# Kernel optimization log

Measured on AMD Instinct MI355X. Metric: run time of the kernel, lower is better.

## Reference

```python
import jax, jax.numpy as jnp
import numpy as np
from jax import lax

DN = ('NCHW', 'OIHW', 'NCHW')

def _conv(x, w, b, pad):
    y = lax.conv_general_dilated(x, w, (1, 1), pad, dimension_numbers=DN)
    return y + b[None, :, None, None]

def _squash(u, eps=1e-8):
    sn = jnp.sum(u * u, axis=1, keepdims=True)  # channel-dim squared norm
    return (sn / (1.0 + sn)) * u / (jnp.sqrt(sn) + eps)

def _expert(x, w_caps, b_caps, w_proj, b_proj):
    # 16 stacked 3x3 capsule convs == one 3x3 conv 128->128 (same concat order)
    u = _conv(x, w_caps, b_caps, 'SAME')
    u = _squash(u)
    return _conv(u, w_proj, b_proj, [(0, 0), (0, 0)])

def _process_gate(x, expert_all, g, top):
    B = x.shape[0]
    x0 = x.mean(axis=(2, 3))                          # [B, C] GAP
    gate_out = jax.nn.softmax(x0 @ g, axis=1)         # [B, E]
    usage = gate_out.sum(0)                           # [E]
    tw, ti = lax.top_k(gate_out, top)                 # [B, top]
    tw = jax.nn.softmax(tw, axis=1)
    sel = expert_all[ti, jnp.arange(B)[:, None]]      # [B, top, C, H, W]
    y = jnp.sum(sel * tw[:, :, None, None, None], axis=1)
    loss = jnp.var(usage, ddof=1) / (usage.mean() ** 2 + 1e-10)
    return y, loss

def setup_inputs() -> dict:
    key = jax.random.key(0)
    ks = jax.random.split(key, 8)
    B, C, H, W, E = 8, 128, 64, 64, 8
    fan_g = 1.0 / np.sqrt(C)
    return {
        'x': jax.random.normal(ks[0], (B, C, H, W), jnp.float32),
        'gate1': jax.random.normal(ks[1], (C, E), jnp.float32) * fan_g,
        'gate2': jax.random.normal(ks[2], (C, E), jnp.float32) * fan_g,
        'gate3': jax.random.normal(ks[3], (C, E), jnp.float32) * fan_g,
        'gate4': jax.random.normal(ks[4], (C, E), jnp.float32) * fan_g,
        'W_caps': jax.random.normal(ks[5], (E, C, C, 3, 3), jnp.float32) * (1.0 / np.sqrt(C * 9)),
        'b_caps': jnp.zeros((E, C), jnp.float32),
        'W_proj': jax.random.normal(ks[6], (E, C, C, 1, 1), jnp.float32) * (1.0 / np.sqrt(C)),
        'b_proj': jnp.zeros((E, C), jnp.float32),
    }

def reference(x, gate1, gate2, gate3, gate4, W_caps, b_caps, W_proj, b_proj):
    top = 2
    # Expert outputs are gate-independent: compute each expert on the full batch once.
    expert_all = jax.vmap(lambda wc, bc, wp, bp: _expert(x, wc, bc, wp, bp))(
        W_caps, b_caps, W_proj, b_proj)      # [E, B, C, H, W]
    y1, l1 = _process_gate(x, expert_all, gate1, top)
    y2, l2 = _process_gate(x, expert_all, gate2, top)
    y3, l3 = _process_gate(x, expert_all, gate3, top)
    y4, l4 = _process_gate(x, expert_all, gate4, top)
    return (y1, y2, y3, y4, l1 + l2 + l3 + l4)
```

## Files before the change

kernel.cpp:

```cpp
#include <hip/hip_runtime.h>
#include <math.h>

#define B_   8
#define C_   128
#define E_   8
#define HW_  4096

typedef unsigned short u16;
typedef unsigned int   u32;
typedef __attribute__((ext_vector_type(8))) short bf16x8;
typedef __attribute__((ext_vector_type(4))) float f32x4;

__device__ __forceinline__ u16 f2bf(float f) {
  u32 u = __float_as_uint(f);
  u32 r = (u + 0x7fffu + ((u >> 16) & 1u)) >> 16;
  return (u16)r;
}
__device__ __forceinline__ float bf2f(u16 h) {
  return __uint_as_float(((u32)h) << 16);
}
__device__ __forceinline__ void gld_lds16(const u16* g, u16* l) {
  __builtin_amdgcn_global_load_lds((const __attribute__((address_space(1))) u32*)g,
                                   (__attribute__((address_space(3))) u32*)(void*)l,
                                   16, 0, 0);
}
#define MFMA(a, b, c) __builtin_amdgcn_mfma_f32_16x16x32_bf16(a, b, c, 0, 0, 0)

__global__ __launch_bounds__(256) void k_mean(const float* __restrict__ x,
                                              float* __restrict__ x0) {
  int bc = blockIdx.x;
  const float4* p = (const float4*)(x + (size_t)bc * HW_);
  float s = 0.f;
  for (int i = threadIdx.x; i < HW_ / 4; i += 256) {
    float4 v = p[i];
    s += v.x + v.y + v.z + v.w;
  }
#pragma unroll
  for (int off = 32; off > 0; off >>= 1) s += __shfl_down(s, off);
  __shared__ float red[4];
  if ((threadIdx.x & 63) == 0) red[threadIdx.x >> 6] = s;
  __syncthreads();
  if (threadIdx.x == 0)
    x0[bc] = (red[0] + red[1] + red[2] + red[3]) * (1.f / HW_);
}

__global__ __launch_bounds__(256) void k_gate(const float* __restrict__ x0,
    const float* __restrict__ g1, const float* __restrict__ g2,
    const float* __restrict__ g3, const float* __restrict__ g4,
    float* __restrict__ wmat, float* __restrict__ w2, int* __restrict__ idxb,
    int* __restrict__ needed, float* __restrict__ lossp) {
  __shared__ float go[4][8][8];
  int t = threadIdx.x;
  int g = t >> 6, b = (t >> 3) & 7, e = t & 7;
  const float* gp = (g == 0) ? g1 : (g == 1) ? g2 : (g == 2) ? g3 : g4;
  const float* xr = x0 + b * C_;
  float s = 0.f;
  for (int c = 0; c < C_; ++c) s += xr[c] * gp[c * E_ + e];
  go[g][b][e] = s;
  wmat[t] = 0.f;
  if (t < 64) needed[t] = 0;
  __syncthreads();
  if (t < 32) {
    int gg = t >> 3, bb = t & 7;
    float m = -1e30f;
#pragma unroll
    for (int k = 0; k < 8; ++k) m = fmaxf(m, go[gg][bb][k]);
    float tmp[8]; float sum = 0.f;
#pragma unroll
    for (int k = 0; k < 8; ++k) { tmp[k] = expf(go[gg][bb][k] - m); sum += tmp[k]; }
    float inv = 1.f / sum;
#pragma unroll
    for (int k = 0; k < 8; ++k) { tmp[k] *= inv; go[gg][bb][k] = tmp[k]; }
    float v0 = -1.f; int i0 = 0;
#pragma unroll
    for (int k = 0; k < 8; ++k) if (tmp[k] > v0) { v0 = tmp[k]; i0 = k; }
    float v1 = -1.f; int i1 = 0;
#pragma unroll
    for (int k = 0; k < 8; ++k) if (k != i0 && tmp[k] > v1) { v1 = tmp[k]; i1 = k; }
    float e1 = expf(v1 - v0);
    float w0 = 1.f / (1.f + e1), w1 = e1 / (1.f + e1);
    w2[t * 2] = w0; w2[t * 2 + 1] = w1;
    idxb[t * 2] = i0; idxb[t * 2 + 1] = i1;
    wmat[(gg * 8 + bb) * 8 + i0] = w0;
    wmat[(gg * 8 + bb) * 8 + i1] = w1;
    needed[i0 * 8 + bb] = 1;
    needed[i1 * 8 + bb] = 1;
  }
  __syncthreads();
  if (t == 0) {
    float total = 0.f;
    for (int gg = 0; gg < 4; ++gg) {
      float us[8]; float mean = 0.f;
      for (int k = 0; k < 8; ++k) {
        float u = 0.f;
        for (int bb = 0; bb < 8; ++bb) u += go[gg][bb][k];
        us[k] = u; mean += u;
      }
      mean *= 0.125f;
      float var = 0.f;
      for (int k = 0; k < 8; ++k) { float d = us[k] - mean; var += d * d; }
      var *= (1.f / 7.f);
      total += var / (mean * mean + 1e-10f);
    }
    *lossp = total;
  }
}

__global__ __launch_bounds__(256) void k_prepx(const float* __restrict__ x,
                                               u16* __restrict__ XTh,
                                               u16* __restrict__ XTl) {
  int y = blockIdx.x;
  int b = blockIdx.y;
  __shared__ float T[64 * 129];
  for (int i = threadIdx.x; i < 128 * 64; i += 256) {
    int ci = i >> 6, xc = i & 63;
    T[xc * 129 + ci] = x[((size_t)(b * 128 + ci)) * HW_ + y * 64 + xc];
  }
  __syncthreads();
  for (int i = threadIdx.x; i < 64 * 128; i += 256) {
    int xc = i >> 7, ci = i & 127;
    float v = T[xc * 129 + ci];
    u16 h = f2bf(v);
    size_t o = ((size_t)(b * HW_ + y * 64 + xc)) * 128 + ci;
    XTh[o] = h;
    XTl[o] = f2bf(v - bf2f(h));
  }
}

__global__ __launch_bounds__(256) void k_prepw(const float* __restrict__ Wc,
    const float* __restrict__ Wp, u16* __restrict__ Wph, u16* __restrict__ Wpl,
    u16* __restrict__ Pph, u16* __restrict__ Ppl) {
  int gid = blockIdx.x * 256 + threadIdx.x;
  int stride = gridDim.x * 256;
  const int N1 = 8 * 9 * 2 * 128 * 64;
  for (int g = gid; g < N1; g += stride) {
    int k = g & 63;
    int co = (g >> 6) & 127;
    int ch = (g >> 13) & 1;
    int v = g >> 14;
    int tap = v % 9, e = v / 9;
    int ci = ch * 64 + k;
    float wv = Wc[(((size_t)(e * 128 + co)) * 128 + ci) * 9 + tap];
    u16 h = f2bf(wv), lo = f2bf(wv - bf2f(h));
    int idx = (v * 2 + ch) * 8192 + co * 64 + (k ^ ((co & 7) << 3));
    Wph[idx] = h; Wpl[idx] = lo;
  }
  const int N2 = 8 * 4 * 128 * 32;
  for (int g = gid; g < N2; g += stride) {
    int k = g & 31;
    int co = (g >> 5) & 127;
    int c = (g >> 12) & 3;
    int e = g >> 14;
    int ci = c * 32 + k;
    float wv = Wp[((size_t)(e * 128 + co)) * 128 + ci];
    u16 h = f2bf(wv), lo = f2bf(wv - bf2f(h));
    int idx = (e * 4 + c) * 4096 + co * 32 + (k ^ ((co & 3) << 3));
    Pph[idx] = h; Ppl[idx] = lo;
  }
}

__global__ __launch_bounds__(256, 2) void k_expert(
    const u16* __restrict__ XTh, const u16* __restrict__ XTl,
    const u16* __restrict__ Wph, const u16* __restrict__ Wpl,
    const u16* __restrict__ Pph, const u16* __restrict__ Ppl,
    const float* __restrict__ bcap, const float* __restrict__ bproj,
    const int* __restrict__ needed, const float* __restrict__ wmat,
    float* __restrict__ expb, float* __restrict__ yout, int use_exp) {
  int e = blockIdx.z, b = blockIdx.y;
  if (!needed[e * 8 + b]) return;
  int tile = blockIdx.x;
  int y0 = tile * 2;

  __shared__ __align__(16) char smem[75264];
  u16* S = (u16*)smem;
  const int Ah = 0, Al = 8192, Bh = 16384, Bl = 24576;
  const int Vh = 0, Vl = 16384, Pt = 32768;
  float* snb = (float*)(smem + 73728);
  float* fb  = (float*)(smem + 74752);

  int tid = threadIdx.x;
  int lane = tid & 63, w = tid >> 6;
  int l15 = lane & 15, l4 = lane >> 4;
  int cob = (w >> 1) * 64, nb = (w & 1) * 64;

  f32x4 zero4 = {0.f, 0.f, 0.f, 0.f};
  f32x4 acc[4][4];
#pragma unroll
  for (int i = 0; i < 4; ++i)
#pragma unroll
    for (int j = 0; j < 4; ++j) acc[i][j] = zero4;

  int sn_ = tid >> 1;
  int kh = (tid & 1) * 4;
  int srow = y0 + (sn_ >> 6);
  int scol = sn_ & 63;

  for (int tap = 0; tap < 9; ++tap) {
    int dy = tap / 3 - 1, dx = tap % 3 - 1;
    int row = srow + dy, col = scol + dx;
    bool val = ((unsigned)row < 64u) && ((unsigned)col < 64u);
    int gidx = val ? ((b * HW_ + row * 64 + col) * 128) : 0;
    for (int ch = 0; ch < 2; ++ch) {
      __syncthreads();
      const u16* wsh = Wph + (size_t)(((e * 9 + tap) * 2 + ch)) * 8192;
      const u16* wsl = Wpl + (size_t)(((e * 9 + tap) * 2 + ch)) * 8192;
#pragma unroll
      for (int q = 0; q < 4; ++q) {
        int off = (w * 4 + q) * 512;
        gld_lds16(wsh + off + lane * 8, S + Ah + off);
        gld_lds16(wsl + off + lane * 8, S + Al + off);
      }
      int ci0 = ch * 64;
#pragma unroll
      for (int i = 0; i < 4; ++i) {
        int kg = kh + i;
        uint4 vh4 = {0u, 0u, 0u, 0u}, vl4 = {0u, 0u, 0u, 0u};
        if (val) {
          vh4 = *(const uint4*)(XTh + gidx + ci0 + kg * 8);
          vl4 = *(const uint4*)(XTl + gidx + ci0 + kg * 8);
        }
        int wa = sn_ * 64 + ((kg * 8) ^ ((sn_ & 7) << 3));
        *(uint4*)(S + Bh + wa) = vh4;
        *(uint4*)(S + Bl + wa) = vl4;
      }
      __syncthreads();
#pragma unroll
      for (int ks = 0; ks < 2; ++ks) {
        bf16x8 fah[4], fal[4], fbh[4], fbl[4];
#pragma unroll
        for (int i = 0; i < 4; ++i) {
          int co = cob + i * 16 + l15;
          int ka = (ks * 32 + l4 * 8) ^ ((co & 7) << 3);
          fah[i] = *(const bf16x8*)(S + Ah + co * 64 + ka);
          fal[i] = *(const bf16x8*)(S + Al + co * 64 + ka);
        }
#pragma unroll
        for (int j = 0; j < 4; ++j) {
          int pn = nb + j * 16 + l15;
          int kb = (ks * 32 + l4 * 8) ^ ((pn & 7) << 3);
          fbh[j] = *(const bf16x8*)(S + Bh + pn * 64 + kb);
          fbl[j] = *(const bf16x8*)(S + Bl + pn * 64 + kb);
        }
#pragma unroll
        for (int i = 0; i < 4; ++i)
#pragma unroll
          for (int j = 0; j < 4; ++j) {
            acc[i][j] = MFMA(fah[i], fbh[j], acc[i][j]);
            acc[i][j] = MFMA(fah[i], fbl[j], acc[i][j]);
            acc[i][j] = MFMA(fal[i], fbh[j], acc[i][j]);
          }
      }
    }
  }

#pragma unroll
  for (int i = 0; i < 4; ++i)
#pragma unroll
    for (int r = 0; r < 4; ++r) {
      float bc = bcap[e * 128 + cob + i * 16 + l4 * 4 + r];
#pragma unroll
      for (int j = 0; j < 4; ++j) acc[i][j][r] += bc;
    }

#pragma unroll
  for (int j = 0; j < 4; ++j) {
    float p = 0.f;
#pragma unroll
    for (int i = 0; i < 4; ++i)
#pragma unroll
      for (int r = 0; r < 4; ++r) p += acc[i][j][r] * acc[i][j][r];
    p += __shfl_xor(p, 16);
    p += __shfl_xor(p, 32);
    if (lane < 16) snb[(w >> 1) * 128 + nb + j * 16 + lane] = p;
  }
  __syncthreads();
  if (tid < 128) {
    float s2 = snb[tid] + snb[128 + tid];
    fb[tid] = s2 / ((1.f + s2) * (sqrtf(s2) + 1e-8f));
  }
  __syncthreads();

#pragma unroll
  for (int j = 0; j < 4; ++j) {
    int pn = nb + j * 16 + l15;
    float fj = fb[pn];
#pragma unroll
    for (int i = 0; i < 4; ++i) {
      int co0v = cob + i * 16 + l4 * 4;
      float v0 = acc[i][j][0] * fj, v1 = acc[i][j][1] * fj;
      float v2 = acc[i][j][2] * fj, v3 = acc[i][j][3] * fj;
      u16 h0 = f2bf(v0), h1 = f2bf(v1), h2 = f2bf(v2), h3 = f2bf(v3);
      uint2 hp; hp.x = (u32)h0 | ((u32)h1 << 16); hp.y = (u32)h2 | ((u32)h3 << 16);
      u16 q0 = f2bf(v0 - bf2f(h0)), q1 = f2bf(v1 - bf2f(h1));
      u16 q2 = f2bf(v2 - bf2f(h2)), q3 = f2bf(v3 - bf2f(h3));
      uint2 lp; lp.x = (u32)q0 | ((u32)q1 << 16); lp.y = (u32)q2 | ((u32)q3 << 16);
      int ad = pn * 128 + (co0v ^ ((pn & 7) << 3));
      *(uint2*)(S + Vh + ad) = hp;
      *(uint2*)(S + Vl + ad) = lp;
    }
  }

#pragma unroll
  for (int i = 0; i < 4; ++i)
#pragma unroll
    for (int j = 0; j < 4; ++j) acc[i][j] = zero4;

  for (int sp = 0; sp < 2; ++sp) {
    const u16* Psrc = sp ? Ppl : Pph;
    for (int c = 0; c < 4; ++c) {
      __syncthreads();
      const u16* ps = Psrc + (size_t)(e * 4 + c) * 4096;
#pragma unroll
      for (int q = 0; q < 2; ++q) {
        int off = (w * 2 + q) * 512;
        gld_lds16(ps + off + lane * 8, S + Pt + off);
      }
      __syncthreads();
      bf16x8 af[4], bvh[4], bvl[4];
#pragma unroll
      for (int i = 0; i < 4; ++i) {
        int co = cob + i * 16 + l15;
        int ka = (l4 * 8) ^ ((co & 3) << 3);
        af[i] = *(const bf16x8*)(S + Pt + co * 32 + ka);
      }
#pragma unroll
      for (int j = 0; j < 4; ++j) {
        int pn = nb + j * 16 + l15;
        int kb = (c * 32 + l4 * 8) ^ ((pn & 7) << 3);
        bvh[j] = *(const bf16x8*)(S + Vh + pn * 128 + kb);
        bvl[j] = *(const bf16x8*)(S + Vl + pn * 128 + kb);
      }
      if (sp == 0) {
#pragma unroll
        for (int i = 0; i < 4; ++i)
#pragma unroll
          for (int j = 0; j < 4; ++j) {
            acc[i][j] = MFMA(af[i], bvh[j], acc[i][j]);
            acc[i][j] = MFMA(af[i], bvl[j], acc[i][j]);
          }
      } else {
#pragma unroll
        for (int i = 0; i < 4; ++i)
#pragma unroll
          for (int j = 0; j < 4; ++j)
            acc[i][j] = MFMA(af[i], bvh[j], acc[i][j]);
      }
    }
  }

  int posbase = tile * 128;
  if (use_exp) {
    float* ob = expb + ((size_t)((e * 8 + b) * 128)) * HW_;
#pragma unroll
    for (int i = 0; i < 4; ++i)
#pragma unroll
      for (int r = 0; r < 4; ++r) {
        int co = cob + i * 16 + l4 * 4 + r;
        float bp = bproj[e * 128 + co];
#pragma unroll
        for (int j = 0; j < 4; ++j) {
          int p = posbase + nb + j * 16 + l15;
          ob[(size_t)co * HW_ + p] = acc[i][j][r] + bp;
        }
      }
  } else {
    for (int g = 0; g < 4; ++g) {
      float wgt = wmat[(g * 8 + b) * 8 + e];
      if (wgt != 0.f) {
        float* ob = yout + (size_t)(g * 8 + b) * (C_ * HW_);
#pragma unroll
        for (int i = 0; i < 4; ++i)
#pragma unroll
          for (int r = 0; r < 4; ++r) {
            int co = cob + i * 16 + l4 * 4 + r;
            float bp = bproj[e * 128 + co];
#pragma unroll
            for (int j = 0; j < 4; ++j) {
              int p = posbase + nb + j * 16 + l15;
              atomicAdd(&ob[(size_t)co * HW_ + p], wgt * (acc[i][j][r] + bp));
            }
          }
      }
    }
  }
}

__global__ __launch_bounds__(256) void k_combine(const float* __restrict__ expb,
    const int* __restrict__ idxb, const float* __restrict__ w2,
    float* __restrict__ yout) {
  int gb = blockIdx.y;
  int b = gb & 7;
  int i0 = idxb[gb * 2], i1 = idxb[gb * 2 + 1];
  float w0 = w2[gb * 2], w1 = w2[gb * 2 + 1];
  const float4* p0 = (const float4*)(expb + (size_t)(i0 * 8 + b) * (C_ * HW_));
  const float4* p1 = (const float4*)(expb + (size_t)(i1 * 8 + b) * (C_ * HW_));
  float4* o = (float4*)(yout + (size_t)gb * (C_ * HW_));
  for (int i = blockIdx.x * 256 + threadIdx.x; i < C_ * HW_ / 4;
       i += gridDim.x * 256) {
    float4 a = p0[i], c = p1[i];
    float4 r = {w0 * a.x + w1 * c.x, w0 * a.y + w1 * c.y,
                w0 * a.z + w1 * c.z, w0 * a.w + w1 * c.w};
    o[i] = r;
  }
}

extern "C" void kernel_launch(void* const* d_in, const int* in_sizes, int n_in,
                              void* d_out, int out_size, void* d_ws, size_t ws_size,
                              hipStream_t stream) {
  const float* x  = (const float*)d_in[0];
  const float* g1 = (const float*)d_in[1];
  const float* g2 = (const float*)d_in[2];
  const float* g3 = (const float*)d_in[3];
  const float* g4 = (const float*)d_in[4];
  const float* Wc = (const float*)d_in[5];
  const float* bc = (const float*)d_in[6];
  const float* Wp = (const float*)d_in[7];
  const float* bp = (const float*)d_in[8];
  float* out = (float*)d_out;

  const size_t EXPF = (size_t)E_ * B_ * C_ * HW_;
  const size_t XTU  = (size_t)B_ * HW_ * C_;
  const size_t WSU  = (size_t)8 * 9 * 2 * 8192;
  const size_t PSU  = (size_t)8 * 4 * 4096;
  const size_t needB = EXPF * 4 + 2 * XTU * 2 + 2 * WSU * 2 + 2 * PSU * 2 + 8192;
  int use_exp = (ws_size >= needB) ? 1 : 0;

  char* p = (char*)d_ws;
  float* expb = nullptr;
  if (use_exp) { expb = (float*)p; p += EXPF * 4; }
  u16* XTh = (u16*)p; p += XTU * 2;
  u16* XTl = (u16*)p; p += XTU * 2;
  u16* Wph = (u16*)p; p += WSU * 2;
  u16* Wpl = (u16*)p; p += WSU * 2;
  u16* Pph = (u16*)p; p += PSU * 2;
  u16* Ppl = (u16*)p; p += PSU * 2;
  float* x0   = (float*)p; p += 1024 * 4;
  float* wmat = (float*)p; p += 256 * 4;
  float* w2   = (float*)p; p += 64 * 4;
  int*   idxb = (int*)p;   p += 64 * 4;
  int*   needed = (int*)p; p += 64 * 4;

  if (!use_exp)
    hipMemsetAsync(d_out, 0, (size_t)4 * B_ * C_ * HW_ * 4, stream);

  k_mean<<<dim3(B_ * C_), dim3(256), 0, stream>>>(x, x0);
  k_gate<<<dim3(1), dim3(256), 0, stream>>>(x0, g1, g2, g3, g4, wmat, w2, idxb,
                                            needed, out + (size_t)4 * B_ * C_ * HW_);
  k_prepx<<<dim3(64, B_), dim3(256), 0, stream>>>(x, XTh, XTl);
  k_prepw<<<dim3(2048), dim3(256), 0, stream>>>(Wc, Wp, Wph, Wpl, Pph, Ppl);
  k_expert<<<dim3(32, B_, E_), dim3(256), 0, stream>>>(
      XTh, XTl, Wph, Wpl, Pph, Ppl, bc, bp, needed, wmat, expb, out, use_exp);
  if (use_exp)
    k_combine<<<dim3(64, 32), dim3(256), 0, stream>>>(expb, idxb, w2, out);
}
```

Before: 304.0 us.

## Register-prefetch next conv/proj stage to overlap global loads with MFMA

The conv and projection loops in the expert kernel now load the next stage's weight and activation tiles from global memory into registers while the current stage's MFMAs run. This replaces the direct global-to-LDS loads and the two __syncthreads per stage with a register double-buffer using raw s_barrier, sched_barrier and setprio. The x-transpose and weight-packing prep kernels are also merged into one launch. In exchange the kernel carries more registers (16 extra uint4 for the prefetch), which may pressure occupancy under the 256,2 launch bounds, and the barrier and waitcnt ordering is hand-managed.

```diff
diff --git a/kernel.cpp b/kernel.cpp
--- a/kernel.cpp
+++ b/kernel.cpp
@@ -18,11 +18,6 @@
 }
 __device__ __forceinline__ float bf2f(u16 h) {
   return __uint_as_float(((u32)h) << 16);
-}
-__device__ __forceinline__ void gld_lds16(const u16* g, u16* l) {
-  __builtin_amdgcn_global_load_lds((const __attribute__((address_space(1))) u32*)g,
-                                   (__attribute__((address_space(3))) u32*)(void*)l,
-                                   16, 0, 0);
 }
 #define MFMA(a, b, c) __builtin_amdgcn_mfma_f32_16x16x32_bf16(a, b, c, 0, 0, 0)
 
@@ -106,56 +101,56 @@
   }
 }
 
-__global__ __launch_bounds__(256) void k_prepx(const float* __restrict__ x,
-                                               u16* __restrict__ XTh,
-                                               u16* __restrict__ XTl) {
-  int y = blockIdx.x;
-  int b = blockIdx.y;
+__global__ __launch_bounds__(256) void k_prep(const float* __restrict__ x,
+    const float* __restrict__ Wc, const float* __restrict__ Wp,
+    u16* __restrict__ XTh, u16* __restrict__ XTl,
+    u16* __restrict__ Wph, u16* __restrict__ Wpl,
+    u16* __restrict__ Pph, u16* __restrict__ Ppl) {
   __shared__ float T[64 * 129];
-  for (int i = threadIdx.x; i < 128 * 64; i += 256) {
-    int ci = i >> 6, xc = i & 63;
-    T[xc * 129 + ci] = x[((size_t)(b * 128 + ci)) * HW_ + y * 64 + xc];
-  }
-  __syncthreads();
-  for (int i = threadIdx.x; i < 64 * 128; i += 256) {
-    int xc = i >> 7, ci = i & 127;
-    float v = T[xc * 129 + ci];
-    u16 h = f2bf(v);
-    size_t o = ((size_t)(b * HW_ + y * 64 + xc)) * 128 + ci;
-    XTh[o] = h;
-    XTl[o] = f2bf(v - bf2f(h));
-  }
-}
-
-__global__ __launch_bounds__(256) void k_prepw(const float* __restrict__ Wc,
-    const float* __restrict__ Wp, u16* __restrict__ Wph, u16* __restrict__ Wpl,
-    u16* __restrict__ Pph, u16* __restrict__ Ppl) {
-  int gid = blockIdx.x * 256 + threadIdx.x;
-  int stride = gridDim.x * 256;
-  const int N1 = 8 * 9 * 2 * 128 * 64;
-  for (int g = gid; g < N1; g += stride) {
-    int k = g & 63;
-    int co = (g >> 6) & 127;
-    int ch = (g >> 13) & 1;
-    int v = g >> 14;
-    int tap = v % 9, e = v / 9;
-    int ci = ch * 64 + k;
-    float wv = Wc[(((size_t)(e * 128 + co)) * 128 + ci) * 9 + tap];
-    u16 h = f2bf(wv), lo = f2bf(wv - bf2f(h));
-    int idx = (v * 2 + ch) * 8192 + co * 64 + (k ^ ((co & 7) << 3));
-    Wph[idx] = h; Wpl[idx] = lo;
-  }
-  const int N2 = 8 * 4 * 128 * 32;
-  for (int g = gid; g < N2; g += stride) {
-    int k = g & 31;
-    int co = (g >> 5) & 127;
-    int c = (g >> 12) & 3;
-    int e = g >> 14;
-    int ci = c * 32 + k;
-    float wv = Wp[((size_t)(e * 128 + co)) * 128 + ci];
-    u16 h = f2bf(wv), lo = f2bf(wv - bf2f(h));
-    int idx = (e * 4 + c) * 4096 + co * 32 + (k ^ ((co & 3) << 3));
-    Pph[idx] = h; Ppl[idx] = lo;
+  int blk = blockIdx.x;
+  if (blk < 512) {
+    int y = blk & 63, b = blk >> 6;
+    for (int i = threadIdx.x; i < 128 * 64; i += 256) {
+      int ci = i >> 6, xc = i & 63;
+      T[xc * 129 + ci] = x[((size_t)(b * 128 + ci)) * HW_ + y * 64 + xc];
+    }
+    __syncthreads();
+    for (int i = threadIdx.x; i < 64 * 128; i += 256) {
+      int xc = i >> 7, ci = i & 127;
+      float v = T[xc * 129 + ci];
+      u16 h = f2bf(v);
+      size_t o = ((size_t)(b * HW_ + y * 64 + xc)) * 128 + ci;
+      XTh[o] = h;
+      XTl[o] = f2bf(v - bf2f(h));
+    }
+  } else {
+    int gid = (blk - 512) * 256 + threadIdx.x;
+    int stride = 1024 * 256;
+    const int N1 = 8 * 9 * 2 * 128 * 64;
+    for (int g = gid; g < N1; g += stride) {
+      int k = g & 63;
+      int co = (g >> 6) & 127;
+      int ch = (g >> 13) & 1;
+      int v = g >> 14;
+      int tap = v % 9, e = v / 9;
+      int ci = ch * 64 + k;
+      float wv = Wc[(((size_t)(e * 128 + co)) * 128 + ci) * 9 + tap];
+      u16 h = f2bf(wv), lo = f2bf(wv - bf2f(h));
+      int idx = (v * 2 + ch) * 8192 + co * 64 + (k ^ ((co & 7) << 3));
+      Wph[idx] = h; Wpl[idx] = lo;
+    }
+    const int N2 = 8 * 4 * 128 * 32;
+    for (int g = gid; g < N2; g += stride) {
+      int k = g & 31;
+      int co = (g >> 5) & 127;
+      int c = (g >> 12) & 3;
+      int e = g >> 14;
+      int ci = c * 32 + k;
+      float wv = Wp[((size_t)(e * 128 + co)) * 128 + ci];
+      u16 h = f2bf(wv), lo = f2bf(wv - bf2f(h));
+      int idx = (e * 4 + c) * 4096 + co * 32 + (k ^ ((co & 3) << 3));
+      Pph[idx] = h; Ppl[idx] = lo;
+    }
   }
 }
 
@@ -195,62 +190,91 @@
   int srow = y0 + (sn_ >> 6);
   int scol = sn_ & 63;
 
-  for (int tap = 0; tap < 9; ++tap) {
-    int dy = tap / 3 - 1, dx = tap % 3 - 1;
-    int row = srow + dy, col = scol + dx;
-    bool val = ((unsigned)row < 64u) && ((unsigned)col < 64u);
-    int gidx = val ? ((b * HW_ + row * 64 + col) * 128) : 0;
-    for (int ch = 0; ch < 2; ++ch) {
-      __syncthreads();
-      const u16* wsh = Wph + (size_t)(((e * 9 + tap) * 2 + ch)) * 8192;
-      const u16* wsl = Wpl + (size_t)(((e * 9 + tap) * 2 + ch)) * 8192;
-#pragma unroll
-      for (int q = 0; q < 4; ++q) {
-        int off = (w * 4 + q) * 512;
-        gld_lds16(wsh + off + lane * 8, S + Ah + off);
-        gld_lds16(wsl + off + lane * 8, S + Al + off);
+  const u16* WphE = Wph + (size_t)e * 9 * 2 * 8192 + tid * 8;
+  const u16* WplE = Wpl + (size_t)e * 9 * 2 * 8192 + tid * 8;
+
+  uint4 ra[8];
+  uint4 rb[8];
+
+#define PREFETCH_CONV(S_)                                                   \
+  {                                                                         \
+    int tap = (S_) >> 1, ch = (S_) & 1;                                     \
+    const u16* wsh = WphE + (tap * 2 + ch) * 8192;                          \
+    const u16* wsl = WplE + (tap * 2 + ch) * 8192;                          \
+    _Pragma("unroll")                                                       \
+    for (int q = 0; q < 4; ++q) {                                           \
+      ra[q]     = *(const uint4*)(wsh + q * 2048);                          \
+      ra[4 + q] = *(const uint4*)(wsl + q * 2048);                          \
+    }                                                                       \
+    int dy = tap / 3 - 1, dx = tap % 3 - 1;                                 \
+    int row = srow + dy, col = scol + dx;                                   \
+    bool val = ((unsigned)row < 64u) && ((unsigned)col < 64u);              \
+    uint4 z4 = {0u, 0u, 0u, 0u};                                            \
+    _Pragma("unroll")                                                       \
+    for (int i = 0; i < 8; ++i) rb[i] = z4;                                 \
+    if (val) {                                                              \
+      int gb_ = (b * HW_ + row * 64 + col) * 128 + ch * 64 + kh * 8;        \
+      _Pragma("unroll")                                                     \
+      for (int i = 0; i < 4; ++i) {                                         \
+        rb[i]     = *(const uint4*)(XTh + gb_ + i * 8);                     \
+        rb[4 + i] = *(const uint4*)(XTl + gb_ + i * 8);                     \
+      }                                                                     \
+    }                                                                       \
+  }
+
+  PREFETCH_CONV(0);
+
+  for (int s = 0; s < 18; ++s) {
+    __builtin_amdgcn_s_barrier();
+#pragma unroll
+    for (int q = 0; q < 4; ++q) {
+      *(uint4*)(S + Ah + q * 2048 + tid * 8) = ra[q];
+      *(uint4*)(S + Al + q * 2048 + tid * 8) = ra[4 + q];
+    }
+#pragma unroll
+    for (int i = 0; i < 4; ++i) {
+      int kg = kh + i;
+      int wa = sn_ * 64 + ((kg * 8) ^ ((sn_ & 7) << 3));
+      *(uint4*)(S + Bh + wa) = rb[i];
+      *(uint4*)(S + Bl + wa) = rb[4 + i];
+    }
+    __builtin_amdgcn_sched_barrier(0);
+    {
+      int sn2 = (s < 17) ? s + 1 : 17;
+      PREFETCH_CONV(sn2);
+    }
+    __builtin_amdgcn_sched_barrier(0);
+    asm volatile("s_waitcnt lgkmcnt(0)" ::: "memory");
+    __builtin_amdgcn_s_barrier();
+    __builtin_amdgcn_sched_barrier(0);
+    __builtin_amdgcn_s_setprio(1);
+#pragma unroll
+    for (int ks = 0; ks < 2; ++ks) {
+      bf16x8 fah[4], fal[4], fbh[4], fbl[4];
+#pragma unroll
+      for (int i = 0; i < 4; ++i) {
+        int co = cob + i * 16 + l15;
+        int ka = (ks * 32 + l4 * 8) ^ ((co & 7) << 3);
+        fah[i] = *(const bf16x8*)(S + Ah + co * 64 + ka);
+        fal[i] = *(const bf16x8*)(S + Al + co * 64 + ka);
       }
-      int ci0 = ch * 64;
-#pragma unroll
-      for (int i = 0; i < 4; ++i) {
-        int kg = kh + i;
-        uint4 vh4 = {0u, 0u, 0u, 0u}, vl4 = {0u, 0u, 0u, 0u};
-        if (val) {
-          vh4 = *(const uint4*)(XTh + gidx + ci0 + kg * 8);
-          vl4 = *(const uint4*)(XTl + gidx + ci0 + kg * 8);
+#pragma unroll
+      for (int j = 0; j < 4; ++j) {
+        int pn = nb + j * 16 + l15;
+        int kb = (ks * 32 + l4 * 8) ^ ((pn & 7) << 3);
+        fbh[j] = *(const bf16x8*)(S + Bh + pn * 64 + kb);
+        fbl[j] = *(const bf16x8*)(S + Bl + pn * 64 + kb);
+      }
+#pragma unroll
+      for (int i = 0; i < 4; ++i)
+#pragma unroll
+        for (int j = 0; j < 4; ++j) {
+          acc[i][j] = MFMA(fah[i], fbh[j], acc[i][j]);
+          acc[i][j] = MFMA(fah[i], fbl[j], acc[i][j]);
+          acc[i][j] = MFMA(fal[i], fbh[j], acc[i][j]);
         }
-        int wa = sn_ * 64 + ((kg * 8) ^ ((sn_ & 7) << 3));
-        *(uint4*)(S + Bh + wa) = vh4;
-        *(uint4*)(S + Bl + wa) = vl4;
-      }
-      __syncthreads();
-#pragma unroll
-      for (int ks = 0; ks < 2; ++ks) {
-        bf16x8 fah[4], fal[4], fbh[4], fbl[4];
-#pragma unroll
-        for (int i = 0; i < 4; ++i) {
-          int co = cob + i * 16 + l15;
-          int ka = (ks * 32 + l4 * 8) ^ ((co & 7) << 3);
-          fah[i] = *(const bf16x8*)(S + Ah + co * 64 + ka);
-          fal[i] = *(const bf16x8*)(S + Al + co * 64 + ka);
-        }
-#pragma unroll
-        for (int j = 0; j < 4; ++j) {
-          int pn = nb + j * 16 + l15;
-          int kb = (ks * 32 + l4 * 8) ^ ((pn & 7) << 3);
-          fbh[j] = *(const bf16x8*)(S + Bh + pn * 64 + kb);
-          fbl[j] = *(const bf16x8*)(S + Bl + pn * 64 + kb);
-        }
-#pragma unroll
-        for (int i = 0; i < 4; ++i)
-#pragma unroll
-          for (int j = 0; j < 4; ++j) {
-            acc[i][j] = MFMA(fah[i], fbh[j], acc[i][j]);
-            acc[i][j] = MFMA(fah[i], fbl[j], acc[i][j]);
-            acc[i][j] = MFMA(fal[i], fbh[j], acc[i][j]);
-          }
-      }
-    }
+    }
+    __builtin_amdgcn_s_setprio(0);
   }
 
 #pragma unroll
@@ -305,47 +329,62 @@
 #pragma unroll
     for (int j = 0; j < 4; ++j) acc[i][j] = zero4;
 
-  for (int sp = 0; sp < 2; ++sp) {
-    const u16* Psrc = sp ? Ppl : Pph;
-    for (int c = 0; c < 4; ++c) {
-      __syncthreads();
-      const u16* ps = Psrc + (size_t)(e * 4 + c) * 4096;
-#pragma unroll
-      for (int q = 0; q < 2; ++q) {
-        int off = (w * 2 + q) * 512;
-        gld_lds16(ps + off + lane * 8, S + Pt + off);
-      }
-      __syncthreads();
-      bf16x8 af[4], bvh[4], bvl[4];
-#pragma unroll
-      for (int i = 0; i < 4; ++i) {
-        int co = cob + i * 16 + l15;
-        int ka = (l4 * 8) ^ ((co & 3) << 3);
-        af[i] = *(const bf16x8*)(S + Pt + co * 32 + ka);
-      }
-#pragma unroll
-      for (int j = 0; j < 4; ++j) {
-        int pn = nb + j * 16 + l15;
-        int kb = (c * 32 + l4 * 8) ^ ((pn & 7) << 3);
-        bvh[j] = *(const bf16x8*)(S + Vh + pn * 128 + kb);
-        bvl[j] = *(const bf16x8*)(S + Vl + pn * 128 + kb);
-      }
-      if (sp == 0) {
-#pragma unroll
-        for (int i = 0; i < 4; ++i)
-#pragma unroll
-          for (int j = 0; j < 4; ++j) {
-            acc[i][j] = MFMA(af[i], bvh[j], acc[i][j]);
-            acc[i][j] = MFMA(af[i], bvl[j], acc[i][j]);
-          }
-      } else {
-#pragma unroll
-        for (int i = 0; i < 4; ++i)
-#pragma unroll
-          for (int j = 0; j < 4; ++j)
-            acc[i][j] = MFMA(af[i], bvh[j], acc[i][j]);
-      }
-    }
+  uint4 rp0, rp1;
+#define PREFETCH_PROJ(ST_)                                                  \
+  {                                                                         \
+    int sp_ = (ST_) >> 2, c_ = (ST_) & 3;                                   \
+    const u16* ps = (sp_ ? Ppl : Pph) + (size_t)(e * 4 + c_) * 4096 +       \
+                    (w * 2) * 512 + lane * 8;                               \
+    rp0 = *(const uint4*)ps;                                                \
+    rp1 = *(const uint4*)(ps + 512);                                        \
+  }
+
+  PREFETCH_PROJ(0);
+  for (int st = 0; st < 8; ++st) {
+    __builtin_amdgcn_s_barrier();
+    *(uint4*)(S + Pt + (w * 2) * 512 + lane * 8) = rp0;
+    *(uint4*)(S + Pt + (w * 2 + 1) * 512 + lane * 8) = rp1;
+    __builtin_amdgcn_sched_barrier(0);
+    {
+      int st2 = (st < 7) ? st + 1 : 7;
+      PREFETCH_PROJ(st2);
+    }
+    __builtin_amdgcn_sched_barrier(0);
+    asm volatile("s_waitcnt lgkmcnt(0)" ::: "memory");
+    __builtin_amdgcn_s_barrier();
+    __builtin_amdgcn_sched_barrier(0);
+    int sp = st >> 2, c = st & 3;
+    bf16x8 af[4], bvh[4], bvl[4];
+#pragma unroll
+    for (int i = 0; i < 4; ++i) {
+      int co = cob + i * 16 + l15;
+      int ka = (l4 * 8) ^ ((co & 3) << 3);
+      af[i] = *(const bf16x8*)(S + Pt + co * 32 + ka);
+    }
+#pragma unroll
+    for (int j = 0; j < 4; ++j) {
+      int pn = nb + j * 16 + l15;
+      int kb = (c * 32 + l4 * 8) ^ ((pn & 7) << 3);
+      bvh[j] = *(const bf16x8*)(S + Vh + pn * 128 + kb);
+      bvl[j] = *(const bf16x8*)(S + Vl + pn * 128 + kb);
+    }
+    __builtin_amdgcn_s_setprio(1);
+    if (sp == 0) {
+#pragma unroll
+      for (int i = 0; i < 4; ++i)
+#pragma unroll
+        for (int j = 0; j < 4; ++j) {
+          acc[i][j] = MFMA(af[i], bvh[j], acc[i][j]);
+          acc[i][j] = MFMA(af[i], bvl[j], acc[i][j]);
+        }
+    } else {
+#pragma unroll
+      for (int i = 0; i < 4; ++i)
+#pragma unroll
+        for (int j = 0; j < 4; ++j)
+          acc[i][j] = MFMA(af[i], bvh[j], acc[i][j]);
+    }
+    __builtin_amdgcn_s_setprio(0);
   }
 
   int posbase = tile * 128;
@@ -383,6 +422,8 @@
       }
     }
   }
+#undef PREFETCH_CONV
+#undef PREFETCH_PROJ
 }
 
 __global__ __launch_bounds__(256) void k_combine(const float* __restrict__ expb,
@@ -446,8 +487,8 @@
   k_mean<<<dim3(B_ * C_), dim3(256), 0, stream>>>(x, x0);
   k_gate<<<dim3(1), dim3(256), 0, stream>>>(x0, g1, g2, g3, g4, wmat, w2, idxb,
                                             needed, out + (size_t)4 * B_ * C_ * HW_);
-  k_prepx<<<dim3(64, B_), dim3(256), 0, stream>>>(x, XTh, XTl);
-  k_prepw<<<dim3(2048), dim3(256), 0, stream>>>(Wc, Wp, Wph, Wpl, Pph, Ppl);
+  k_prep<<<dim3(1536), dim3(256), 0, stream>>>(x, Wc, Wp, XTh, XTl, Wph, Wpl,
+                                               Pph, Ppl);
   k_expert<<<dim3(32, B_, E_), dim3(256), 0, stream>>>(
       XTh, XTl, Wph, Wpl, Pph, Ppl, bc, bp, needed, wmat, expb, out, use_exp);
   if (use_exp)
```

Result: slower. 456.7 us (+50.2%).

## Fuse mean into prep kernel and scatter expert outputs via atomics directly

Applied to the files above, without the earlier changes.

Merges the GAP mean, x transpose/split, and weight prep into one launch, with the mean computed from the staged tile and accumulated atomically. Drops the full expert buffer and the combine kernel. Each expert block now atomically adds its weighted output into every gate's result that selected it, after zeroing the output with a memset. This removes a large intermediate write and read plus launches, but relies on many float atomics, which make summation order nondeterministic. It also adds a barrier before the projection stage.

```diff
diff --git a/kernel.cpp b/kernel.cpp
--- a/kernel.cpp
+++ b/kernel.cpp
@@ -26,29 +26,11 @@
 }
 #define MFMA(a, b, c) __builtin_amdgcn_mfma_f32_16x16x32_bf16(a, b, c, 0, 0, 0)
 
-__global__ __launch_bounds__(256) void k_mean(const float* __restrict__ x,
-                                              float* __restrict__ x0) {
-  int bc = blockIdx.x;
-  const float4* p = (const float4*)(x + (size_t)bc * HW_);
-  float s = 0.f;
-  for (int i = threadIdx.x; i < HW_ / 4; i += 256) {
-    float4 v = p[i];
-    s += v.x + v.y + v.z + v.w;
-  }
-#pragma unroll
-  for (int off = 32; off > 0; off >>= 1) s += __shfl_down(s, off);
-  __shared__ float red[4];
-  if ((threadIdx.x & 63) == 0) red[threadIdx.x >> 6] = s;
-  __syncthreads();
-  if (threadIdx.x == 0)
-    x0[bc] = (red[0] + red[1] + red[2] + red[3]) * (1.f / HW_);
-}
-
 __global__ __launch_bounds__(256) void k_gate(const float* __restrict__ x0,
     const float* __restrict__ g1, const float* __restrict__ g2,
     const float* __restrict__ g3, const float* __restrict__ g4,
-    float* __restrict__ wmat, float* __restrict__ w2, int* __restrict__ idxb,
-    int* __restrict__ needed, float* __restrict__ lossp) {
+    float* __restrict__ wmat, int* __restrict__ needed,
+    float* __restrict__ lossp) {
   __shared__ float go[4][8][8];
   int t = threadIdx.x;
   int g = t >> 6, b = (t >> 3) & 7, e = t & 7;
@@ -56,6 +38,7 @@
   const float* xr = x0 + b * C_;
   float s = 0.f;
   for (int c = 0; c < C_; ++c) s += xr[c] * gp[c * E_ + e];
+  s *= (1.f / 4096.f);
   go[g][b][e] = s;
   wmat[t] = 0.f;
   if (t < 64) needed[t] = 0;
@@ -79,8 +62,6 @@
     for (int k = 0; k < 8; ++k) if (k != i0 && tmp[k] > v1) { v1 = tmp[k]; i1 = k; }
     float e1 = expf(v1 - v0);
     float w0 = 1.f / (1.f + e1), w1 = e1 / (1.f + e1);
-    w2[t * 2] = w0; w2[t * 2 + 1] = w1;
-    idxb[t * 2] = i0; idxb[t * 2 + 1] = i1;
     wmat[(gg * 8 + bb) * 8 + i0] = w0;
     wmat[(gg * 8 + bb) * 8 + i1] = w1;
     needed[i0 * 8 + bb] = 1;
@@ -106,56 +87,62 @@
   }
 }
 
-__global__ __launch_bounds__(256) void k_prepx(const float* __restrict__ x,
-                                               u16* __restrict__ XTh,
-                                               u16* __restrict__ XTl) {
-  int y = blockIdx.x;
-  int b = blockIdx.y;
+__global__ __launch_bounds__(256) void k_prep(const float* __restrict__ x,
+    const float* __restrict__ Wc, const float* __restrict__ Wp,
+    u16* __restrict__ XTh, u16* __restrict__ XTl,
+    u16* __restrict__ Wph, u16* __restrict__ Wpl,
+    u16* __restrict__ Pph, u16* __restrict__ Ppl, float* __restrict__ x0) {
   __shared__ float T[64 * 129];
-  for (int i = threadIdx.x; i < 128 * 64; i += 256) {
-    int ci = i >> 6, xc = i & 63;
-    T[xc * 129 + ci] = x[((size_t)(b * 128 + ci)) * HW_ + y * 64 + xc];
-  }
-  __syncthreads();
-  for (int i = threadIdx.x; i < 64 * 128; i += 256) {
-    int xc = i >> 7, ci = i & 127;
-    float v = T[xc * 129 + ci];
-    u16 h = f2bf(v);
-    size_t o = ((size_t)(b * HW_ + y * 64 + xc)) * 128 + ci;
-    XTh[o] = h;
-    XTl[o] = f2bf(v - bf2f(h));
-  }
-}
-
-__global__ __launch_bounds__(256) void k_prepw(const float* __restrict__ Wc,
-    const float* __restrict__ Wp, u16* __restrict__ Wph, u16* __restrict__ Wpl,
-    u16* __restrict__ Pph, u16* __restrict__ Ppl) {
-  int gid = blockIdx.x * 256 + threadIdx.x;
-  int stride = gridDim.x * 256;
-  const int N1 = 8 * 9 * 2 * 128 * 64;
-  for (int g = gid; g < N1; g += stride) {
-    int k = g & 63;
-    int co = (g >> 6) & 127;
-    int ch = (g >> 13) & 1;
-    int v = g >> 14;
-    int tap = v % 9, e = v / 9;
-    int ci = ch * 64 + k;
-    float wv = Wc[(((size_t)(e * 128 + co)) * 128 + ci) * 9 + tap];
-    u16 h = f2bf(wv), lo = f2bf(wv - bf2f(h));
-    int idx = (v * 2 + ch) * 8192 + co * 64 + (k ^ ((co & 7) << 3));
-    Wph[idx] = h; Wpl[idx] = lo;
-  }
-  const int N2 = 8 * 4 * 128 * 32;
-  for (int g = gid; g < N2; g += stride) {
-    int k = g & 31;
-    int co = (g >> 5) & 127;
-    int c = (g >> 12) & 3;
-    int e = g >> 14;
-    int ci = c * 32 + k;
-    float wv = Wp[((size_t)(e * 128 + co)) * 128 + ci];
-    u16 h = f2bf(wv), lo = f2bf(wv - bf2f(h));
-    int idx = (e * 4 + c) * 4096 + co * 32 + (k ^ ((co & 3) << 3));
-    Pph[idx] = h; Ppl[idx] = lo;
+  int blk = blockIdx.x;
+  if (blk < 512) {
+    int y = blk & 63, b = blk >> 6;
+    for (int i = threadIdx.x; i < 128 * 64; i += 256) {
+      int ci = i >> 6, xc = i & 63;
+      T[xc * 129 + ci] = x[((size_t)(b * 128 + ci)) * HW_ + y * 64 + xc];
+    }
+    __syncthreads();
+    if (threadIdx.x < 128) {
+      int ci = threadIdx.x;
+      float s = 0.f;
+      for (int xc = 0; xc < 64; ++xc) s += T[xc * 129 + ci];
+      atomicAdd(&x0[b * 128 + ci], s);
+    }
+    for (int i = threadIdx.x; i < 64 * 128; i += 256) {
+      int xc = i >> 7, ci = i & 127;
+      float v = T[xc * 129 + ci];
+      u16 h = f2bf(v);
+      size_t o = ((size_t)(b * HW_ + y * 64 + xc)) * 128 + ci;
+      XTh[o] = h;
+      XTl[o] = f2bf(v - bf2f(h));
+    }
+  } else {
+    int gid = (blk - 512) * 256 + threadIdx.x;
+    int stride = 1024 * 256;
+    const int N1 = 8 * 9 * 2 * 128 * 64;
+    for (int g = gid; g < N1; g += stride) {
+      int k = g & 63;
+      int co = (g >> 6) & 127;
+      int ch = (g >> 13) & 1;
+      int v = g >> 14;
+      int tap = v % 9, e = v / 9;
+      int ci = ch * 64 + k;
+      float wv = Wc[(((size_t)(e * 128 + co)) * 128 + ci) * 9 + tap];
+      u16 h = f2bf(wv), lo = f2bf(wv - bf2f(h));
+      int idx = (v * 2 + ch) * 8192 + co * 64 + (k ^ ((co & 7) << 3));
+      Wph[idx] = h; Wpl[idx] = lo;
+    }
+    const int N2 = 8 * 4 * 128 * 32;
+    for (int g = gid; g < N2; g += stride) {
+      int k = g & 31;
+      int co = (g >> 5) & 127;
+      int c = (g >> 12) & 3;
+      int e = g >> 14;
+      int ci = c * 32 + k;
+      float wv = Wp[((size_t)(e * 128 + co)) * 128 + ci];
+      u16 h = f2bf(wv), lo = f2bf(wv - bf2f(h));
+      int idx = (e * 4 + c) * 4096 + co * 32 + (k ^ ((co & 3) << 3));
+      Pph[idx] = h; Ppl[idx] = lo;
+    }
   }
 }
 
@@ -165,7 +152,7 @@
     const u16* __restrict__ Pph, const u16* __restrict__ Ppl,
     const float* __restrict__ bcap, const float* __restrict__ bproj,
     const int* __restrict__ needed, const float* __restrict__ wmat,
-    float* __restrict__ expb, float* __restrict__ yout, int use_exp) {
+    float* __restrict__ yout) {
   int e = blockIdx.z, b = blockIdx.y;
   if (!needed[e * 8 + b]) return;
   int tile = blockIdx.x;
@@ -194,6 +181,9 @@
   int kh = (tid & 1) * 4;
   int srow = y0 + (sn_ >> 6);
   int scol = sn_ & 63;
+
+  const u16* WphE = Wph + (size_t)e * 9 * 2 * 8192;
+  const u16* WplE = Wpl + (size_t)e * 9 * 2 * 8192;
 
   for (int tap = 0; tap < 9; ++tap) {
     int dy = tap / 3 - 1, dx = tap % 3 - 1;
@@ -202,8 +192,8 @@
     int gidx = val ? ((b * HW_ + row * 64 + col) * 128) : 0;
     for (int ch = 0; ch < 2; ++ch) {
       __syncthreads();
-      const u16* wsh = Wph + (size_t)(((e * 9 + tap) * 2 + ch)) * 8192;
-      const u16* wsl = Wpl + (size_t)(((e * 9 + tap) * 2 + ch)) * 8192;
+      const u16* wsh = WphE + (tap * 2 + ch) * 8192;
+      const u16* wsl = WplE + (tap * 2 + ch) * 8192;
 #pragma unroll
       for (int q = 0; q < 4; ++q) {
         int off = (w * 4 + q) * 512;
@@ -299,6 +289,7 @@
       *(uint2*)(S + Vl + ad) = lp;
     }
   }
+  __syncthreads();
 
 #pragma unroll
   for (int i = 0; i < 4; ++i)
@@ -349,59 +340,31 @@
   }
 
   int posbase = tile * 128;
-  if (use_exp) {
-    float* ob = expb + ((size_t)((e * 8 + b) * 128)) * HW_;
-#pragma unroll
-    for (int i = 0; i < 4; ++i)
-#pragma unroll
-      for (int r = 0; r < 4; ++r) {
-        int co = cob + i * 16 + l4 * 4 + r;
-        float bp = bproj[e * 128 + co];
-#pragma unroll
-        for (int j = 0; j < 4; ++j) {
-          int p = posbase + nb + j * 16 + l15;
-          ob[(size_t)co * HW_ + p] = acc[i][j][r] + bp;
-        }
-      }
-  } else {
-    for (int g = 0; g < 4; ++g) {
-      float wgt = wmat[(g * 8 + b) * 8 + e];
-      if (wgt != 0.f) {
-        float* ob = yout + (size_t)(g * 8 + b) * (C_ * HW_);
-#pragma unroll
-        for (int i = 0; i < 4; ++i)
-#pragma unroll
-          for (int r = 0; r < 4; ++r) {
-            int co = cob + i * 16 + l4 * 4 + r;
-            float bp = bproj[e * 128 + co];
-#pragma unroll
-            for (int j = 0; j < 4; ++j) {
-              int p = posbase + nb + j * 16 + l15;
-              atomicAdd(&ob[(size_t)co * HW_ + p], wgt * (acc[i][j][r] + bp));
-            }
-          }
-      }
-    }
-  }
-}
-
-__global__ __launch_bounds__(256) void k_combine(const float* __restrict__ expb,
-    const int* __restrict__ idxb, const float* __restrict__ w2,
-    float* __restrict__ yout) {
-  int gb = blockIdx.y;
-  int b = gb & 7;
-  int i0 = idxb[gb * 2], i1 = idxb[gb * 2 + 1];
-  float w0 = w2[gb * 2], w1 = w2[gb * 2 + 1];
-  const float4* p0 = (const float4*)(expb + (size_t)(i0 * 8 + b) * (C_ * HW_));
-  const float4* p1 = (const float4*)(expb + (size_t)(i1 * 8 + b) * (C_ * HW_));
-  float4* o = (float4*)(yout + (size_t)gb * (C_ * HW_));
-  for (int i = blockIdx.x * 256 + threadIdx.x; i < C_ * HW_ / 4;
-       i += gridDim.x * 256) {
-    float4 a = p0[i], c = p1[i];
-    float4 r = {w0 * a.x + w1 * c.x, w0 * a.y + w1 * c.y,
-                w0 * a.z + w1 * c.z, w0 * a.w + w1 * c.w};
-    o[i] = r;
-  }
+  float wg0 = wmat[(0 * 8 + b) * 8 + e];
+  float wg1 = wmat[(1 * 8 + b) * 8 + e];
+  float wg2 = wmat[(2 * 8 + b) * 8 + e];
+  float wg3 = wmat[(3 * 8 + b) * 8 + e];
+  float* o0 = yout + (size_t)(0 * 8 + b) * (C_ * HW_);
+  float* o1 = yout + (size_t)(1 * 8 + b) * (C_ * HW_);
+  float* o2 = yout + (size_t)(2 * 8 + b) * (C_ * HW_);
+  float* o3 = yout + (size_t)(3 * 8 + b) * (C_ * HW_);
+#pragma unroll
+  for (int i = 0; i < 4; ++i)
+#pragma unroll
+    for (int r = 0; r < 4; ++r) {
+      int co = cob + i * 16 + l4 * 4 + r;
+      float bp = bproj[e * 128 + co];
+      size_t rowo = (size_t)co * HW_ + posbase;
+#pragma unroll
+      for (int j = 0; j < 4; ++j) {
+        int p = nb + j * 16 + l15;
+        float v = acc[i][j][r] + bp;
+        if (wg0 != 0.f) atomicAdd(o0 + rowo + p, wg0 * v);
+        if (wg1 != 0.f) atomicAdd(o1 + rowo + p, wg1 * v);
+        if (wg2 != 0.f) atomicAdd(o2 + rowo + p, wg2 * v);
+        if (wg3 != 0.f) atomicAdd(o3 + rowo + p, wg3 * v);
+      }
+    }
 }
 
 extern "C" void kernel_launch(void* const* d_in, const int* in_sizes, int n_in,
@@ -418,16 +381,11 @@
   const float* bp = (const float*)d_in[8];
   float* out = (float*)d_out;
 
-  const size_t EXPF = (size_t)E_ * B_ * C_ * HW_;
   const size_t XTU  = (size_t)B_ * HW_ * C_;
   const size_t WSU  = (size_t)8 * 9 * 2 * 8192;
   const size_t PSU  = (size_t)8 * 4 * 4096;
-  const size_t needB = EXPF * 4 + 2 * XTU * 2 + 2 * WSU * 2 + 2 * PSU * 2 + 8192;
-  int use_exp = (ws_size >= needB) ? 1 : 0;
 
   char* p = (char*)d_ws;
-  float* expb = nullptr;
-  if (use_exp) { expb = (float*)p; p += EXPF * 4; }
   u16* XTh = (u16*)p; p += XTU * 2;
   u16* XTl = (u16*)p; p += XTU * 2;
   u16* Wph = (u16*)p; p += WSU * 2;
@@ -436,20 +394,15 @@
   u16* Ppl = (u16*)p; p += PSU * 2;
   float* x0   = (float*)p; p += 1024 * 4;
   float* wmat = (float*)p; p += 256 * 4;
-  float* w2   = (float*)p; p += 64 * 4;
-  int*   idxb = (int*)p;   p += 64 * 4;
   int*   needed = (int*)p; p += 64 * 4;
 
-  if (!use_exp)
-    hipMemsetAsync(d_out, 0, (size_t)4 * B_ * C_ * HW_ * 4, stream);
-
-  k_mean<<<dim3(B_ * C_), dim3(256), 0, stream>>>(x, x0);
-  k_gate<<<dim3(1), dim3(256), 0, stream>>>(x0, g1, g2, g3, g4, wmat, w2, idxb,
-                                            needed, out + (size_t)4 * B_ * C_ * HW_);
-  k_prepx<<<dim3(64, B_), dim3(256), 0, stream>>>(x, XTh, XTl);
-  k_prepw<<<dim3(2048), dim3(256), 0, stream>>>(Wc, Wp, Wph, Wpl, Pph, Ppl);
+  hipMemsetAsync(out, 0, (size_t)4 * B_ * C_ * HW_ * 4, stream);
+  hipMemsetAsync(x0, 0, 1024 * 4, stream);
+
+  k_prep<<<dim3(1536), dim3(256), 0, stream>>>(x, Wc, Wp, XTh, XTl, Wph, Wpl,
+                                               Pph, Ppl, x0);
+  k_gate<<<dim3(1), dim3(256), 0, stream>>>(x0, g1, g2, g3, g4, wmat, needed,
+                                            out + (size_t)4 * B_ * C_ * HW_);
   k_expert<<<dim3(32, B_, E_), dim3(256), 0, stream>>>(
-      XTh, XTl, Wph, Wpl, Pph, Ppl, bc, bp, needed, wmat, expb, out, use_exp);
-  if (use_exp)
-    k_combine<<<dim3(64, 32), dim3(256), 0, stream>>>(expb, idxb, w2, out);
-}
+      XTh, XTl, Wph, Wpl, Pph, Ppl, bc, bp, needed, wmat, out);
+}
```

After: 347.4 us. 1.14x slower.
